# Kernel optimization log

Measured on AMD Instinct MI355X. Metric: run time of the kernel, lower is better.

Reference implementation:

```python
import jax, jax.numpy as jnp
import numpy as np

SEQ_LEN = 4096
HID = 2048      # hidden_dim == input_dim
NF = 512        # n_features


def setup_inputs() -> dict:
    key = jax.random.key(0)
    ks = jax.random.split(key, 13)
    s = 0.02
    return {
        "x": jax.random.normal(ks[0], (1, 1, NF), jnp.float32),
        "input_hidden": jax.random.normal(ks[1], (1, 1, HID), jnp.float32),
        "input_cell": jax.random.normal(ks[2], (1, 1, HID), jnp.float32),
        "encoder_outputs": jax.random.normal(ks[3], (1, SEQ_LEN, HID), jnp.float32),
        # Bahdanau attention params: Linear(2H -> H) and scoring vector v
        "W_attn": jax.random.normal(ks[4], (HID, 2 * HID), jnp.float32) * s,
        "b_attn": jnp.zeros((HID,), jnp.float32),
        "v_attn": jax.random.normal(ks[5], (HID,), jnp.float32) * s,
        # LSTM params (PyTorch layout, gate order i,f,g,o), input size = H + NF
        "W_ih": jax.random.normal(ks[6], (4 * HID, HID + NF), jnp.float32) * s,
        "W_hh": jax.random.normal(ks[7], (4 * HID, HID), jnp.float32) * s,
        "b_ih": jnp.zeros((4 * HID,), jnp.float32),
        "b_hh": jnp.zeros((4 * HID,), jnp.float32),
        # output Linear(2H -> NF)
        "W_out": jax.random.normal(ks[8], (NF, 2 * HID), jnp.float32) * s,
        "b_out": jnp.zeros((NF,), jnp.float32),
    }


def reference(x, input_hidden, input_cell, encoder_outputs,
              W_attn, b_attn, v_attn, W_ih, W_hh, b_ih, b_hh, W_out, b_out):
    # ---- attention(input_hidden, encoder_outputs) -> a: [B, S] ----
    h_last = input_hidden[-1]                      # [B, H]
    B, S, H = encoder_outputs.shape
    h_rep = jnp.broadcast_to(h_last[:, None, :], (B, S, H))
    energy = jnp.tanh(jnp.concatenate([h_rep, encoder_outputs], axis=-1) @ W_attn.T + b_attn)
    scores = jnp.einsum('bsh,h->bs', energy, v_attn)
    a = jax.nn.softmax(scores, axis=1)             # [B, S]

    # weighted = bmm(a.unsqueeze(1), encoder_outputs) -> [B, H]
    weighted = jnp.einsum('bs,bsh->bh', a, encoder_outputs)

    # ---- single-step LSTM (num_layers=1, batch_first) ----
    rnn_in = jnp.concatenate([x.reshape(1, -1), weighted], axis=-1)  # [1, NF+H]
    h0 = input_hidden[0]                           # [1, H]
    c0 = input_cell[0]                             # [1, H]
    gates = rnn_in @ W_ih.T + b_ih + h0 @ W_hh.T + b_hh  # [1, 4H]
    i, f, g, o = jnp.split(gates, 4, axis=-1)
    c_n = jax.nn.sigmoid(f) * c0 + jax.nn.sigmoid(i) * jnp.tanh(g)
    h_n = jax.nn.sigmoid(o) * jnp.tanh(c_n)        # [1, H] == output.squeeze(0)

    # ---- output projection on cat(output, weighted) ----
    out = jnp.concatenate([h_n, weighted], axis=-1) @ W_out.T + b_out  # [1, NF]
    return out, h_n[None], c_n[None]
```

## Files before the change

### kernel.cpp

```cpp
#include <hip/hip_runtime.h>
#include <hip/hip_bf16.h>
#include <math.h>


#define HIDDEN 2048
#define SEQL   4096
#define NFEAT  512

typedef __attribute__((ext_vector_type(8))) short frag_t;
typedef __attribute__((ext_vector_type(8))) unsigned short u16x8;
typedef __attribute__((ext_vector_type(4))) float f32x4;

__device__ __forceinline__ unsigned short f2bf(float f) {
    union { float f; unsigned int u; } c; c.f = f;
    unsigned int r = c.u + 0x7fffu + ((c.u >> 16) & 1u);
    return (unsigned short)(r >> 16);
}

__device__ __forceinline__ float wave_sum(float s) {
    #pragma unroll
    for (int off = 32; off; off >>= 1) s += __shfl_down(s, off);
    return s;
}

__device__ __forceinline__ void gload16(const unsigned short* g, unsigned short* l) {
    __builtin_amdgcn_global_load_lds(
        (const __attribute__((address_space(1))) unsigned int*)g,
        (__attribute__((address_space(3))) unsigned int*)l, 16, 0, 0);
}

__global__ __launch_bounds__(256)
void k_conv(const float* __restrict__ enc, const float* __restrict__ Wattn,
            unsigned short* __restrict__ encbf, unsigned short* __restrict__ wbf)
{
    const int b = blockIdx.x;
    const float* src;
    unsigned short* dst;
    if (b < 4096) {
        src = enc + (size_t)b * 2048;
        dst = encbf + (size_t)b * 2048;
    } else {
        const int r = b - 4096;
        src = Wattn + (size_t)r * 4096 + 2048;
        dst = wbf + (size_t)r * 2048;
    }
    const int t = threadIdx.x;
    float4 a = *reinterpret_cast<const float4*>(src + t * 8);
    float4 c = *reinterpret_cast<const float4*>(src + t * 8 + 4);
    u16x8 o;
    o[0] = f2bf(a.x); o[1] = f2bf(a.y); o[2] = f2bf(a.z); o[3] = f2bf(a.w);
    o[4] = f2bf(c.x); o[5] = f2bf(c.y); o[6] = f2bf(c.z); o[7] = f2bf(c.w);
    *reinterpret_cast<u16x8*>(dst + t * 8) = o;
}

__global__ __launch_bounds__(256)
void k_pre_gemv(const float* __restrict__ Wattn, const float* __restrict__ b_attn,
                const float* __restrict__ Wih,  const float* __restrict__ Whh,
                const float* __restrict__ b_ih, const float* __restrict__ b_hh,
                const float* __restrict__ x,    const float* __restrict__ h0,
                float* __restrict__ h_pre, float* __restrict__ gates)
{
    const int gw = (blockIdx.x * 256 + threadIdx.x) >> 6;
    const int lane = threadIdx.x & 63;
    if (gw < HIDDEN) {
        const float* Wr = Wattn + (size_t)gw * 4096;
        float s = 0.f;
        #pragma unroll
        for (int i = 0; i < 8; i++) {
            int c = i * 256 + lane * 4;
            float4 wv = *reinterpret_cast<const float4*>(Wr + c);
            float4 hv = *reinterpret_cast<const float4*>(h0 + c);
            s += wv.x*hv.x + wv.y*hv.y + wv.z*hv.z + wv.w*hv.w;
        }
        s = wave_sum(s);
        if (lane == 0) h_pre[gw] = s + b_attn[gw];
    } else {
        const int j = gw - HIDDEN;
        const float* W1 = Wih + (size_t)j * 2560;
        const float* W2 = Whh + (size_t)j * 2048;
        float s = 0.f;
        #pragma unroll
        for (int i = 0; i < 2; i++) {
            int c = i * 256 + lane * 4;
            float4 wv = *reinterpret_cast<const float4*>(W1 + c);
            float4 xv = *reinterpret_cast<const float4*>(x + c);
            s += wv.x*xv.x + wv.y*xv.y + wv.z*xv.z + wv.w*xv.w;
        }
        #pragma unroll
        for (int i = 0; i < 8; i++) {
            int c = i * 256 + lane * 4;
            float4 wv = *reinterpret_cast<const float4*>(W2 + c);
            float4 hv = *reinterpret_cast<const float4*>(h0 + c);
            s += wv.x*hv.x + wv.y*hv.y + wv.z*hv.z + wv.w*hv.w;
        }
        s = wave_sum(s);
        if (lane == 0) gates[j] = s + b_ih[j] + b_hh[j];
    }
}

__global__ __launch_bounds__(256)
void k_energy2(const unsigned short* __restrict__ encbf,
               const unsigned short* __restrict__ wbf,
               const float* __restrict__ h_pre, const float* __restrict__ v_attn,
               float* __restrict__ pscore)
{
    __shared__ __align__(16) unsigned short As[128 * 64];
    __shared__ __align__(16) unsigned short Bs[128 * 64];
    __shared__ float sh_hv[2][128];
    __shared__ float sh_part[2][128];

    const int tid = threadIdx.x;
    const int hb = blockIdx.x;
    const int sb = blockIdx.y;
    const int s0 = sb * 128, h0 = hb * 128;
    const int wv = tid >> 6, lane = tid & 63;
    const int wm = wv >> 1, wn = wv & 1;

    const unsigned short* srcA[4];
    const unsigned short* srcB[4];
    #pragma unroll
    for (int i = 0; i < 4; i++) {
        const int c = wv * 4 + i;
        const int row = c * 8 + (lane >> 3);
        const int k0 = ((lane & 7) ^ (row & 7)) * 8;
        srcA[i] = encbf + (size_t)(s0 + row) * 2048 + k0;
        srcB[i] = wbf  + (size_t)(h0 + row) * 2048 + k0;
    }

    f32x4 acc[4][4];
    #pragma unroll
    for (int m = 0; m < 4; m++)
        #pragma unroll
        for (int n = 0; n < 4; n++)
            acc[m][n] = (f32x4){0.f, 0.f, 0.f, 0.f};

    const int swz = (lane & 7) << 4;
    const int hi16 = (lane >> 4) * 16;

    for (int kt = 0; kt < 2048; kt += 64) {
        __syncthreads();
        #pragma unroll
        for (int i = 0; i < 4; i++) {
            const int c = wv * 4 + i;
            gload16(srcA[i] + kt, &As[c * 512]);
            gload16(srcB[i] + kt, &Bs[c * 512]);
        }
        __syncthreads();

        frag_t af[2][4], bq[2][4];
        #pragma unroll
        for (int ks = 0; ks < 2; ks++) {
            const int lo = (ks * 64 + hi16) ^ swz;
            #pragma unroll
            for (int m = 0; m < 4; m++) {
                const int rowa = wm * 64 + m * 16 + (lane & 15);
                af[ks][m] = *reinterpret_cast<const frag_t*>(
                    reinterpret_cast<const char*>(As) + rowa * 128 + lo);
                const int rowb = wn * 64 + m * 16 + (lane & 15);
                bq[ks][m] = *reinterpret_cast<const frag_t*>(
                    reinterpret_cast<const char*>(Bs) + rowb * 128 + lo);
            }
        }
        #pragma unroll
        for (int ks = 0; ks < 2; ks++)
            #pragma unroll
            for (int m = 0; m < 4; m++)
                #pragma unroll
                for (int n = 0; n < 4; n++)
                    acc[m][n] = __builtin_amdgcn_mfma_f32_16x16x32_bf16(
                        af[ks][m], bq[ks][n], acc[m][n], 0, 0, 0);
    }

    if (tid < 128) { sh_hv[0][tid] = h_pre[h0 + tid]; sh_hv[1][tid] = v_attn[h0 + tid]; }
    __syncthreads();

    float ps[4][4];
    #pragma unroll
    for (int m = 0; m < 4; m++)
        #pragma unroll
        for (int r = 0; r < 4; r++) ps[m][r] = 0.f;

    #pragma unroll
    for (int m = 0; m < 4; m++) {
        #pragma unroll
        for (int n = 0; n < 4; n++) {
            const int hc = wn * 64 + n * 16 + (lane & 15);
            const float hp = sh_hv[0][hc], vvv = sh_hv[1][hc];
            #pragma unroll
            for (int r = 0; r < 4; r++) {
                float e = tanhf(acc[m][n][r] + hp);
                ps[m][r] += e * vvv;
            }
        }
    }
    #pragma unroll
    for (int m = 0; m < 4; m++)
        #pragma unroll
        for (int r = 0; r < 4; r++) {
            float p = ps[m][r];
            #pragma unroll
            for (int off = 1; off < 16; off <<= 1) p += __shfl_xor(p, off);
            ps[m][r] = p;
        }
    if ((lane & 15) == 0) {
        const int grp = lane >> 4;
        #pragma unroll
        for (int m = 0; m < 4; m++)
            #pragma unroll
            for (int r = 0; r < 4; r++)
                sh_part[wn][wm * 64 + m * 16 + grp * 4 + r] = ps[m][r];
    }
    __syncthreads();
    if (tid < 128)
        pscore[hb * SEQL + s0 + tid] = sh_part[0][tid] + sh_part[1][tid];
}

__global__ __launch_bounds__(1024)
void k_softmax(const float* __restrict__ pscore, float* __restrict__ attnw)
{
    __shared__ float red[16];
    __shared__ float bcast;
    const int t = threadIdx.x, wv = t >> 6, lane = t & 63;
    float s[4];
    #pragma unroll
    for (int q = 0; q < 4; q++) {
        const int idx = q * 1024 + t;
        float a = 0.f;
        #pragma unroll
        for (int p = 0; p < 16; p++) a += pscore[p * SEQL + idx];
        s[q] = a;
    }
    float mx = fmaxf(fmaxf(s[0], s[1]), fmaxf(s[2], s[3]));
    #pragma unroll
    for (int off = 32; off; off >>= 1) mx = fmaxf(mx, __shfl_xor(mx, off));
    if (!lane) red[wv] = mx;
    __syncthreads();
    if (t == 0) {
        float m = red[0];
        for (int i = 1; i < 16; i++) m = fmaxf(m, red[i]);
        bcast = m;
    }
    __syncthreads();
    const float bm = bcast;
    float e[4], sum = 0.f;
    #pragma unroll
    for (int q = 0; q < 4; q++) { e[q] = __expf(s[q] - bm); sum += e[q]; }
    #pragma unroll
    for (int off = 32; off; off >>= 1) sum += __shfl_xor(sum, off);
    __syncthreads();
    if (!lane) red[wv] = sum;
    __syncthreads();
    if (t == 0) {
        float m = 0.f;
        for (int i = 0; i < 16; i++) m += red[i];
        bcast = m;
    }
    __syncthreads();
    const float inv = 1.f / bcast;
    #pragma unroll
    for (int q = 0; q < 4; q++) attnw[q * 1024 + t] = e[q] * inv;
}

__global__ __launch_bounds__(256)
void k_weighted_part(const float* __restrict__ enc, const float* __restrict__ attnw,
                     float* __restrict__ pweight)
{
    const int hb = blockIdx.x & 7, sbk = blockIdx.x >> 3;
    const int h = hb * 256 + threadIdx.x;
    const int sbase = sbk * 64;
    float acc = 0.f;
    for (int s = 0; s < 64; s++)
        acc += attnw[sbase + s] * enc[(size_t)(sbase + s) * HIDDEN + h];
    pweight[sbk * HIDDEN + h] = acc;
}

__global__ __launch_bounds__(256)
void k_weighted_reduce(const float* __restrict__ pweight, float* __restrict__ weighted)
{
    const int h = blockIdx.x * 256 + threadIdx.x;
    float acc = 0.f;
    #pragma unroll 8
    for (int sb = 0; sb < 64; sb++) acc += pweight[sb * HIDDEN + h];
    weighted[h] = acc;
}

__global__ __launch_bounds__(256)
void k_gates_fin(const float* __restrict__ Wih, const float* __restrict__ weighted,
                 float* __restrict__ gates)
{
    const int j = (blockIdx.x * 256 + threadIdx.x) >> 6;
    const int lane = threadIdx.x & 63;
    const float* Wr = Wih + (size_t)j * 2560 + 512;
    float s = 0.f;
    #pragma unroll
    for (int i = 0; i < 8; i++) {
        int c = i * 256 + lane * 4;
        float4 wv = *reinterpret_cast<const float4*>(Wr + c);
        float4 hv = *reinterpret_cast<const float4*>(weighted + c);
        s += wv.x*hv.x + wv.y*hv.y + wv.z*hv.z + wv.w*hv.w;
    }
    s = wave_sum(s);
    if (lane == 0) gates[j] += s;
}

__global__ __launch_bounds__(256)
void k_lstm(const float* __restrict__ gates, const float* __restrict__ c0,
            float* __restrict__ dout)
{
    const int t = blockIdx.x * 256 + threadIdx.x;
    const float gi = gates[t];
    const float gf = gates[2048 + t];
    const float gg = gates[4096 + t];
    const float go = gates[6144 + t];
    const float si = 1.f / (1.f + __expf(-gi));
    const float sf = 1.f / (1.f + __expf(-gf));
    const float so = 1.f / (1.f + __expf(-go));
    const float c = sf * c0[t] + si * tanhf(gg);
    const float h = so * tanhf(c);
    dout[512 + t]  = h;
    dout[2560 + t] = c;
}

__global__ __launch_bounds__(256)
void k_out_gemv(const float* __restrict__ Wout, const float* __restrict__ b_out,
                const float* __restrict__ hn, const float* __restrict__ weighted,
                float* __restrict__ dout)
{
    const int n = (blockIdx.x * 256 + threadIdx.x) >> 6;
    const int lane = threadIdx.x & 63;
    const float* Wr = Wout + (size_t)n * 4096;
    float s = 0.f;
    #pragma unroll
    for (int i = 0; i < 8; i++) {
        int c = i * 256 + lane * 4;
        float4 wv = *reinterpret_cast<const float4*>(Wr + c);
        float4 hv = *reinterpret_cast<const float4*>(hn + c);
        s += wv.x*hv.x + wv.y*hv.y + wv.z*hv.z + wv.w*hv.w;
        float4 wv2 = *reinterpret_cast<const float4*>(Wr + 2048 + c);
        float4 hv2 = *reinterpret_cast<const float4*>(weighted + c);
        s += wv2.x*hv2.x + wv2.y*hv2.y + wv2.z*hv2.z + wv2.w*hv2.w;
    }
    s = wave_sum(s);
    if (lane == 0) dout[n] = s + b_out[n];
}

extern "C" void kernel_launch(void* const* d_in, const int* in_sizes, int n_in,
                              void* d_out, int out_size, void* d_ws, size_t ws_size,
                              hipStream_t stream)
{
    const float* x        = (const float*)d_in[0];
    const float* ih       = (const float*)d_in[1];
    const float* ic       = (const float*)d_in[2];
    const float* enc      = (const float*)d_in[3];
    const float* Wattn    = (const float*)d_in[4];
    const float* b_attn   = (const float*)d_in[5];
    const float* v_attn   = (const float*)d_in[6];
    const float* Wih      = (const float*)d_in[7];
    const float* Whh      = (const float*)d_in[8];
    const float* b_ih     = (const float*)d_in[9];
    const float* b_hh     = (const float*)d_in[10];
    const float* Wout     = (const float*)d_in[11];
    const float* b_out    = (const float*)d_in[12];
    float* dout = (float*)d_out;

    unsigned short* encbf = (unsigned short*)d_ws;
    unsigned short* wbf   = encbf + (size_t)8388608;
    float* wsf      = (float*)(wbf + (size_t)4194304);
    float* h_pre    = wsf;
    float* gates    = wsf + 2048;
    float* pscore   = wsf + 10240;
    float* attnw    = wsf + 75776;
    float* pweight  = wsf + 79872;
    float* weighted = wsf + 210944;

    k_conv<<<6144, 256, 0, stream>>>(enc, Wattn, encbf, wbf);
    k_pre_gemv<<<2560, 256, 0, stream>>>(Wattn, b_attn, Wih, Whh, b_ih, b_hh,
                                         x, ih, h_pre, gates);
    k_energy2<<<dim3(16, 32), 256, 0, stream>>>(encbf, wbf, h_pre, v_attn, pscore);
    k_softmax<<<1, 1024, 0, stream>>>(pscore, attnw);
    k_weighted_part<<<512, 256, 0, stream>>>(enc, attnw, pweight);
    k_weighted_reduce<<<8, 256, 0, stream>>>(pweight, weighted);
    k_gates_fin<<<2048, 256, 0, stream>>>(Wih, weighted, gates);
    k_lstm<<<8, 256, 0, stream>>>(gates, ic, dout);
    k_out_gemv<<<128, 256, 0, stream>>>(Wout, b_out, dout + 512, weighted, dout);
}
```

Measured before the change: 109.5 us.

## Fuse GEMV stages into conversion, energy and gate kernels; read bf16 encoder for weighting

Folds the attention h_pre GEMV into the bf16 conversion kernel and the LSTM hidden/x gate GEMV into extra blocks of the energy MFMA kernel. The separate gate-finish, LSTM and output kernels are merged so the weighted half of the output projection runs alongside the gate finish, leaving a small kernel for the h_n half. The weighted-sum pass now reads the bf16 encoder copy instead of fp32, halving its memory traffic. Partial sums are stored over the no-longer-needed W bf16 buffer. This cuts the launch count and overlaps GEMVs with the GEMM, at the cost of bf16 precision in the weighted sum.

```diff
diff --git a/kernel.cpp b/kernel.cpp
--- a/kernel.cpp
+++ b/kernel.cpp
@@ -17,6 +17,11 @@
     return (unsigned short)(r >> 16);
 }
 
+__device__ __forceinline__ float bf2f(unsigned short u) {
+    union { unsigned int u; float f; } c; c.u = (unsigned int)u << 16;
+    return c.f;
+}
+
 __device__ __forceinline__ float wave_sum(float s) {
     #pragma unroll
     for (int off = 32; off; off >>= 1) s += __shfl_down(s, off);
@@ -30,39 +35,33 @@
 }
 
 __global__ __launch_bounds__(256)
-void k_conv(const float* __restrict__ enc, const float* __restrict__ Wattn,
-            unsigned short* __restrict__ encbf, unsigned short* __restrict__ wbf)
+void k_conv_hpre(const float* __restrict__ enc, const float* __restrict__ Wattn,
+                 const float* __restrict__ b_attn, const float* __restrict__ h0,
+                 unsigned short* __restrict__ encbf, unsigned short* __restrict__ wbf,
+                 float* __restrict__ h_pre)
 {
     const int b = blockIdx.x;
-    const float* src;
-    unsigned short* dst;
-    if (b < 4096) {
-        src = enc + (size_t)b * 2048;
-        dst = encbf + (size_t)b * 2048;
+    if (b < 6144) {
+        const float* src;
+        unsigned short* dst;
+        if (b < 4096) {
+            src = enc + (size_t)b * 2048;
+            dst = encbf + (size_t)b * 2048;
+        } else {
+            const int r = b - 4096;
+            src = Wattn + (size_t)r * 4096 + 2048;
+            dst = wbf + (size_t)r * 2048;
+        }
+        const int t = threadIdx.x;
+        float4 a = *reinterpret_cast<const float4*>(src + t * 8);
+        float4 c = *reinterpret_cast<const float4*>(src + t * 8 + 4);
+        u16x8 o;
+        o[0] = f2bf(a.x); o[1] = f2bf(a.y); o[2] = f2bf(a.z); o[3] = f2bf(a.w);
+        o[4] = f2bf(c.x); o[5] = f2bf(c.y); o[6] = f2bf(c.z); o[7] = f2bf(c.w);
+        *reinterpret_cast<u16x8*>(dst + t * 8) = o;
     } else {
-        const int r = b - 4096;
-        src = Wattn + (size_t)r * 4096 + 2048;
-        dst = wbf + (size_t)r * 2048;
-    }
-    const int t = threadIdx.x;
-    float4 a = *reinterpret_cast<const float4*>(src + t * 8);
-    float4 c = *reinterpret_cast<const float4*>(src + t * 8 + 4);
-    u16x8 o;
-    o[0] = f2bf(a.x); o[1] = f2bf(a.y); o[2] = f2bf(a.z); o[3] = f2bf(a.w);
-    o[4] = f2bf(c.x); o[5] = f2bf(c.y); o[6] = f2bf(c.z); o[7] = f2bf(c.w);
-    *reinterpret_cast<u16x8*>(dst + t * 8) = o;
-}
-
-__global__ __launch_bounds__(256)
-void k_pre_gemv(const float* __restrict__ Wattn, const float* __restrict__ b_attn,
-                const float* __restrict__ Wih,  const float* __restrict__ Whh,
-                const float* __restrict__ b_ih, const float* __restrict__ b_hh,
-                const float* __restrict__ x,    const float* __restrict__ h0,
-                float* __restrict__ h_pre, float* __restrict__ gates)
-{
-    const int gw = (blockIdx.x * 256 + threadIdx.x) >> 6;
-    const int lane = threadIdx.x & 63;
-    if (gw < HIDDEN) {
+        const int gw = (b - 6144) * 4 + (threadIdx.x >> 6);
+        const int lane = threadIdx.x & 63;
         const float* Wr = Wattn + (size_t)gw * 4096;
         float s = 0.f;
         #pragma unroll
@@ -74,35 +73,17 @@
         }
         s = wave_sum(s);
         if (lane == 0) h_pre[gw] = s + b_attn[gw];
-    } else {
-        const int j = gw - HIDDEN;
-        const float* W1 = Wih + (size_t)j * 2560;
-        const float* W2 = Whh + (size_t)j * 2048;
-        float s = 0.f;
-        #pragma unroll
-        for (int i = 0; i < 2; i++) {
-            int c = i * 256 + lane * 4;
-            float4 wv = *reinterpret_cast<const float4*>(W1 + c);
-            float4 xv = *reinterpret_cast<const float4*>(x + c);
-            s += wv.x*xv.x + wv.y*xv.y + wv.z*xv.z + wv.w*xv.w;
-        }
-        #pragma unroll
-        for (int i = 0; i < 8; i++) {
-            int c = i * 256 + lane * 4;
-            float4 wv = *reinterpret_cast<const float4*>(W2 + c);
-            float4 hv = *reinterpret_cast<const float4*>(h0 + c);
-            s += wv.x*hv.x + wv.y*hv.y + wv.z*hv.z + wv.w*hv.w;
-        }
-        s = wave_sum(s);
-        if (lane == 0) gates[j] = s + b_ih[j] + b_hh[j];
-    }
-}
-
-__global__ __launch_bounds__(256)
-void k_energy2(const unsigned short* __restrict__ encbf,
-               const unsigned short* __restrict__ wbf,
-               const float* __restrict__ h_pre, const float* __restrict__ v_attn,
-               float* __restrict__ pscore)
+    }
+}
+
+__global__ __launch_bounds__(256)
+void k_energy_gates(const unsigned short* __restrict__ encbf,
+                    const unsigned short* __restrict__ wbf,
+                    const float* __restrict__ h_pre, const float* __restrict__ v_attn,
+                    const float* __restrict__ Wih,  const float* __restrict__ Whh,
+                    const float* __restrict__ b_ih, const float* __restrict__ b_hh,
+                    const float* __restrict__ x,    const float* __restrict__ h0,
+                    float* __restrict__ pscore, float* __restrict__ gates)
 {
     __shared__ __align__(16) unsigned short As[128 * 64];
     __shared__ __align__(16) unsigned short Bs[128 * 64];
@@ -110,10 +91,39 @@
     __shared__ float sh_part[2][128];
 
     const int tid = threadIdx.x;
-    const int hb = blockIdx.x;
-    const int sb = blockIdx.y;
-    const int s0 = sb * 128, h0 = hb * 128;
     const int wv = tid >> 6, lane = tid & 63;
+
+    if (blockIdx.x >= 512) {
+        const int g = blockIdx.x - 512;
+        #pragma unroll
+        for (int r = 0; r < 2; r++) {
+            const int j = g * 8 + wv * 2 + r;
+            const float* W1 = Wih + (size_t)j * 2560;
+            const float* W2 = Whh + (size_t)j * 2048;
+            float s = 0.f;
+            #pragma unroll
+            for (int i = 0; i < 2; i++) {
+                int c = i * 256 + lane * 4;
+                float4 wvv = *reinterpret_cast<const float4*>(W1 + c);
+                float4 xv = *reinterpret_cast<const float4*>(x + c);
+                s += wvv.x*xv.x + wvv.y*xv.y + wvv.z*xv.z + wvv.w*xv.w;
+            }
+            #pragma unroll
+            for (int i = 0; i < 8; i++) {
+                int c = i * 256 + lane * 4;
+                float4 wvv = *reinterpret_cast<const float4*>(W2 + c);
+                float4 hv = *reinterpret_cast<const float4*>(h0 + c);
+                s += wvv.x*hv.x + wvv.y*hv.y + wvv.z*hv.z + wvv.w*hv.w;
+            }
+            s = wave_sum(s);
+            if (lane == 0) gates[j] = s + b_ih[j] + b_hh[j];
+        }
+        return;
+    }
+
+    const int hb = blockIdx.x & 15;
+    const int sb = blockIdx.x >> 4;
+    const int s0 = sb * 128, h0i = hb * 128;
     const int wm = wv >> 1, wn = wv & 1;
 
     const unsigned short* srcA[4];
@@ -124,7 +134,7 @@
         const int row = c * 8 + (lane >> 3);
         const int k0 = ((lane & 7) ^ (row & 7)) * 8;
         srcA[i] = encbf + (size_t)(s0 + row) * 2048 + k0;
-        srcB[i] = wbf  + (size_t)(h0 + row) * 2048 + k0;
+        srcB[i] = wbf  + (size_t)(h0i + row) * 2048 + k0;
     }
 
     f32x4 acc[4][4];
@@ -171,7 +181,7 @@
                         af[ks][m], bq[ks][n], acc[m][n], 0, 0, 0);
     }
 
-    if (tid < 128) { sh_hv[0][tid] = h_pre[h0 + tid]; sh_hv[1][tid] = v_attn[h0 + tid]; }
+    if (tid < 128) { sh_hv[0][tid] = h_pre[h0i + tid]; sh_hv[1][tid] = v_attn[h0i + tid]; }
     __syncthreads();
 
     float ps[4][4];
@@ -262,16 +272,24 @@
 }
 
 __global__ __launch_bounds__(256)
-void k_weighted_part(const float* __restrict__ enc, const float* __restrict__ attnw,
-                     float* __restrict__ pweight)
-{
-    const int hb = blockIdx.x & 7, sbk = blockIdx.x >> 3;
-    const int h = hb * 256 + threadIdx.x;
-    const int sbase = sbk * 64;
-    float acc = 0.f;
-    for (int s = 0; s < 64; s++)
-        acc += attnw[sbase + s] * enc[(size_t)(sbase + s) * HIDDEN + h];
-    pweight[sbk * HIDDEN + h] = acc;
+void k_weighted_part(const unsigned short* __restrict__ encbf,
+                     const float* __restrict__ attnw, float* __restrict__ pweight)
+{
+    const int blk = blockIdx.x;
+    const int t = threadIdx.x;
+    const int sbase = blk * 16;
+    float acc[8];
+    #pragma unroll
+    for (int i = 0; i < 8; i++) acc[i] = 0.f;
+    for (int s = 0; s < 16; s++) {
+        const float a = attnw[sbase + s];
+        u16x8 v = *reinterpret_cast<const u16x8*>(encbf + (size_t)(sbase + s) * 2048 + t * 8);
+        #pragma unroll
+        for (int i = 0; i < 8; i++) acc[i] += a * bf2f(v[i]);
+    }
+    #pragma unroll
+    for (int i = 0; i < 8; i++)
+        pweight[(size_t)blk * 2048 + t * 8 + i] = acc[i];
 }
 
 __global__ __launch_bounds__(256)
@@ -280,50 +298,61 @@
     const int h = blockIdx.x * 256 + threadIdx.x;
     float acc = 0.f;
     #pragma unroll 8
-    for (int sb = 0; sb < 64; sb++) acc += pweight[sb * HIDDEN + h];
+    for (int p = 0; p < 256; p++) acc += pweight[(size_t)p * 2048 + h];
     weighted[h] = acc;
 }
 
 __global__ __launch_bounds__(256)
-void k_gates_fin(const float* __restrict__ Wih, const float* __restrict__ weighted,
-                 float* __restrict__ gates)
-{
-    const int j = (blockIdx.x * 256 + threadIdx.x) >> 6;
-    const int lane = threadIdx.x & 63;
-    const float* Wr = Wih + (size_t)j * 2560 + 512;
-    float s = 0.f;
-    #pragma unroll
-    for (int i = 0; i < 8; i++) {
-        int c = i * 256 + lane * 4;
-        float4 wv = *reinterpret_cast<const float4*>(Wr + c);
-        float4 hv = *reinterpret_cast<const float4*>(weighted + c);
-        s += wv.x*hv.x + wv.y*hv.y + wv.z*hv.z + wv.w*hv.w;
-    }
-    s = wave_sum(s);
-    if (lane == 0) gates[j] += s;
-}
-
-__global__ __launch_bounds__(256)
-void k_lstm(const float* __restrict__ gates, const float* __restrict__ c0,
-            float* __restrict__ dout)
-{
-    const int t = blockIdx.x * 256 + threadIdx.x;
-    const float gi = gates[t];
-    const float gf = gates[2048 + t];
-    const float gg = gates[4096 + t];
-    const float go = gates[6144 + t];
-    const float si = 1.f / (1.f + __expf(-gi));
-    const float sf = 1.f / (1.f + __expf(-gf));
-    const float so = 1.f / (1.f + __expf(-go));
-    const float c = sf * c0[t] + si * tanhf(gg);
-    const float h = so * tanhf(c);
-    dout[512 + t]  = h;
-    dout[2560 + t] = c;
-}
-
-__global__ __launch_bounds__(256)
-void k_out_gemv(const float* __restrict__ Wout, const float* __restrict__ b_out,
-                const float* __restrict__ hn, const float* __restrict__ weighted,
+void k_gates_lstm_outR(const float* __restrict__ Wih, const float* __restrict__ weighted,
+                       const float* __restrict__ gates, const float* __restrict__ c0,
+                       const float* __restrict__ Wout, const float* __restrict__ b_out,
+                       float* __restrict__ dout)
+{
+    __shared__ float sh[4];
+    const int wv = threadIdx.x >> 6, lane = threadIdx.x & 63;
+    if (blockIdx.x < 2048) {
+        const int t = blockIdx.x;
+        const int j = t + 2048 * wv;
+        const float* Wr = Wih + (size_t)j * 2560 + 512;
+        float s = 0.f;
+        #pragma unroll
+        for (int i = 0; i < 8; i++) {
+            int c = i * 256 + lane * 4;
+            float4 wvv = *reinterpret_cast<const float4*>(Wr + c);
+            float4 hv = *reinterpret_cast<const float4*>(weighted + c);
+            s += wvv.x*hv.x + wvv.y*hv.y + wvv.z*hv.z + wvv.w*hv.w;
+        }
+        s = wave_sum(s);
+        if (lane == 0) sh[wv] = s + gates[j];
+        __syncthreads();
+        if (threadIdx.x == 0) {
+            const float gi = sh[0], gf = sh[1], gg = sh[2], go = sh[3];
+            const float si = 1.f / (1.f + __expf(-gi));
+            const float sf = 1.f / (1.f + __expf(-gf));
+            const float so = 1.f / (1.f + __expf(-go));
+            const float c = sf * c0[t] + si * tanhf(gg);
+            const float h = so * tanhf(c);
+            dout[512 + t]  = h;
+            dout[2560 + t] = c;
+        }
+    } else {
+        const int n = (blockIdx.x - 2048) * 4 + wv;
+        const float* Wr = Wout + (size_t)n * 4096 + 2048;
+        float s = 0.f;
+        #pragma unroll
+        for (int i = 0; i < 8; i++) {
+            int c = i * 256 + lane * 4;
+            float4 wvv = *reinterpret_cast<const float4*>(Wr + c);
+            float4 hv = *reinterpret_cast<const float4*>(weighted + c);
+            s += wvv.x*hv.x + wvv.y*hv.y + wvv.z*hv.z + wvv.w*hv.w;
+        }
+        s = wave_sum(s);
+        if (lane == 0) dout[n] = s + b_out[n];
+    }
+}
+
+__global__ __launch_bounds__(256)
+void k_out_left(const float* __restrict__ Wout, const float* __restrict__ hn,
                 float* __restrict__ dout)
 {
     const int n = (blockIdx.x * 256 + threadIdx.x) >> 6;
@@ -336,12 +365,9 @@
         float4 wv = *reinterpret_cast<const float4*>(Wr + c);
         float4 hv = *reinterpret_cast<const float4*>(hn + c);
         s += wv.x*hv.x + wv.y*hv.y + wv.z*hv.z + wv.w*hv.w;
-        float4 wv2 = *reinterpret_cast<const float4*>(Wr + 2048 + c);
-        float4 hv2 = *reinterpret_cast<const float4*>(weighted + c);
-        s += wv2.x*hv2.x + wv2.y*hv2.y + wv2.z*hv2.z + wv2.w*hv2.w;
     }
     s = wave_sum(s);
-    if (lane == 0) dout[n] = s + b_out[n];
+    if (lane == 0) dout[n] += s;
 }
 
 extern "C" void kernel_launch(void* const* d_in, const int* in_sizes, int n_in,
@@ -365,22 +391,22 @@
 
     unsigned short* encbf = (unsigned short*)d_ws;
     unsigned short* wbf   = encbf + (size_t)8388608;
+    float* pweight  = (float*)wbf;
     float* wsf      = (float*)(wbf + (size_t)4194304);
     float* h_pre    = wsf;
     float* gates    = wsf + 2048;
     float* pscore   = wsf + 10240;
     float* attnw    = wsf + 75776;
-    float* pweight  = wsf + 79872;
-    float* weighted = wsf + 210944;
-
-    k_conv<<<6144, 256, 0, stream>>>(enc, Wattn, encbf, wbf);
-    k_pre_gemv<<<2560, 256, 0, stream>>>(Wattn, b_attn, Wih, Whh, b_ih, b_hh,
-                                         x, ih, h_pre, gates);
-    k_energy2<<<dim3(16, 32), 256, 0, stream>>>(encbf, wbf, h_pre, v_attn, pscore);
+    float* weighted = wsf + 79872;
+
+    k_conv_hpre<<<6656, 256, 0, stream>>>(enc, Wattn, b_attn, ih, encbf, wbf, h_pre);
+    k_energy_gates<<<1536, 256, 0, stream>>>(encbf, wbf, h_pre, v_attn,
+                                             Wih, Whh, b_ih, b_hh, x, ih,
+                                             pscore, gates);
     k_softmax<<<1, 1024, 0, stream>>>(pscore, attnw);
-    k_weighted_part<<<512, 256, 0, stream>>>(enc, attnw, pweight);
+    k_weighted_part<<<256, 256, 0, stream>>>(encbf, attnw, pweight);
     k_weighted_reduce<<<8, 256, 0, stream>>>(pweight, weighted);
-    k_gates_fin<<<2048, 256, 0, stream>>>(Wih, weighted, gates);
-    k_lstm<<<8, 256, 0, stream>>>(gates, ic, dout);
-    k_out_gemv<<<128, 256, 0, stream>>>(Wout, b_out, dout + 512, weighted, dout);
-}
+    k_gates_lstm_outR<<<2176, 256, 0, stream>>>(Wih, weighted, gates, ic,
+                                                Wout, b_out, dout);
+    k_out_left<<<128, 256, 0, stream>>>(Wout, dout + 512, dout);
+}
```

Result: no change. 110.1 us (+0.6%).
